# Kernel optimization log

Hardware: AMD Instinct MI355X
Metric: run time of the kernel (lower is better)

## Reference

```python
import jax, jax.numpy as jnp
import numpy as np

N_NODES = 50000
N_EDGES = 800000
IN_DIM = 32
HID = 64
OUT_DIM = 4
HEADS = 4
LAYERS = 3
N_GRAPHS = 50
NEG_SLOPE = 0.2
BN_EPS = 1e-5


def setup_inputs() -> dict:
    key = jax.random.key(0)
    ks = jax.random.split(key, 20)
    x = jax.random.normal(ks[0], (N_NODES, IN_DIM), dtype=jnp.float32)
    edge_index = jax.random.randint(ks[1], (2, N_EDGES), 0, N_NODES, dtype=jnp.int64)
    batch = jnp.sort(jax.random.randint(ks[2], (N_NODES,), 0, N_GRAPHS, dtype=jnp.int64))
    s = 0.05
    inp = {
        "x": x,
        "edge_index": edge_index,
        "batch": batch,
        "in_W": jax.random.normal(ks[3], (IN_DIM, HID), jnp.float32) * s,
        "in_b": jnp.zeros((HID,), jnp.float32),
        "gat_W": jax.random.normal(ks[4], (LAYERS, HID, HEADS * HID), jnp.float32) * s,
        "att_src": jax.random.normal(ks[5], (LAYERS, HEADS, HID), jnp.float32) * s,
        "att_dst": jax.random.normal(ks[6], (LAYERS, HEADS, HID), jnp.float32) * s,
        "gat_b": jnp.zeros((LAYERS, HID), jnp.float32),
        "bn_g": jnp.ones((LAYERS, HID), jnp.float32),
        "bn_b": jnp.zeros((LAYERS, HID), jnp.float32),
        "bn_m": jnp.zeros((LAYERS, HID), jnp.float32),
        "bn_v": jnp.ones((LAYERS, HID), jnp.float32),
        "fc1_W": jax.random.normal(ks[7], (HID, HID), jnp.float32) * s,
        "fc1_b": jnp.zeros((HID,), jnp.float32),
        "fc2_W": jax.random.normal(ks[8], (HID, OUT_DIM), jnp.float32) * s,
        "fc2_b": jnp.zeros((OUT_DIM,), jnp.float32),
    }
    return inp


def _gat_layer(x, src, dst, W, a_src, a_dst, b):
    # x: [N, HID]; src/dst: [E'] (self-loops included)
    N = x.shape[0]
    xt = (x @ W).reshape(N, HEADS, HID)           # [N, H, C]
    sc_src = jnp.einsum("nhc,hc->nh", xt, a_src)  # [N, H]
    sc_dst = jnp.einsum("nhc,hc->nh", xt, a_dst)
    e = jax.nn.leaky_relu(sc_src[src] + sc_dst[dst], NEG_SLOPE)  # [E, H]
    # segment softmax over incoming edges of each dst node
    emax = jax.ops.segment_max(e, dst, num_segments=N)
    ex = jnp.exp(e - emax[dst])
    denom = jax.ops.segment_sum(ex, dst, num_segments=N)
    alpha = ex / (denom[dst] + 1e-16)             # [E, H]
    msg = xt[src] * alpha[:, :, None]             # [E, H, C]
    out = jax.ops.segment_sum(msg, dst, num_segments=N)  # [N, H, C]
    return out.mean(axis=1) + b                   # head-average (concat=False)


def reference(x, edge_index, batch, in_W, in_b, gat_W, att_src, att_dst, gat_b,
              bn_g, bn_b, bn_m, bn_v, fc1_W, fc1_b, fc2_W, fc2_b):
    N = x.shape[0]
    loops = jnp.arange(N, dtype=edge_index.dtype)
    src = jnp.concatenate([edge_index[0], loops])
    dst = jnp.concatenate([edge_index[1], loops])

    h = x @ in_W + in_b  # dropout: eval mode (identity)
    for i in range(LAYERS):
        identity = h
        h = _gat_layer(h, src, dst, gat_W[i], att_src[i], att_dst[i], gat_b[i])
        # BatchNorm1d in eval mode (running stats)
        h = (h - bn_m[i]) * jax.lax.rsqrt(bn_v[i] + BN_EPS) * bn_g[i] + bn_b[i]
        h = jax.nn.relu(h)
        h = h + identity

    # global mean pool over graphs
    sums = jax.ops.segment_sum(h, batch, num_segments=N_GRAPHS)
    cnt = jax.ops.segment_sum(jnp.ones((N,), h.dtype), batch, num_segments=N_GRAPHS)
    g = sums / jnp.maximum(cnt, 1.0)[:, None]     # [N_GRAPHS, HID]

    g = jax.nn.relu(g @ fc1_W + fc1_b)
    return g @ fc2_W + fc2_b                      # [N_GRAPHS, OUT_DIM]
```

## Files before the change

kernel.cpp:

```cpp
#include <hip/hip_runtime.h>
#include <hip/hip_fp16.h>
#include <math.h>

#define HID 64
#define HEADS 4
#define HC 256
#define IN_DIM 32
#define NEG 0.2f
#define BN_EPS 1e-5f
#define CAP 64

typedef _Float16 f16;
typedef _Float16 f16x8 __attribute__((ext_vector_type(8)));
typedef float f32x4 __attribute__((ext_vector_type(4)));

__device__ __forceinline__ int ld_idx(const int* __restrict__ p, int i, int f64) {
    return f64 ? p[(size_t)2 * i] : p[i];
}

__global__ void k_init(const int* __restrict__ ei, int* __restrict__ flag,
                       int* __restrict__ deg, float* __restrict__ gsum,
                       int N, int NG,
                       const float* __restrict__ gat_W, const float* __restrict__ asrc,
                       const float* __restrict__ adst, float* __restrict__ wts,
                       float* __restrict__ wtd, __half* __restrict__ BT) {
    int i = blockIdx.x * blockDim.x + threadIdx.x;
    if (i == 0) {
        int z = 1;
#pragma unroll
        for (int k = 1; k < 64; k += 2) z &= (ei[k] == 0);
        *flag = z;
    }
    if (i < N) deg[i] = 0;
    if (i < NG) gsum[i] = 0.f;
    if (blockIdx.x < 3) {
        int l = blockIdx.x;
        int t = threadIdx.x;
        int hh = t >> 6, k = t & 63;
        {
            const float* W = gat_W + (size_t)l * HID * HC + (size_t)k * HC + hh * HID;
            const float* as = asrc + (size_t)l * HEADS * HID + hh * HID;
            const float* ad = adst + (size_t)l * HEADS * HID + hh * HID;
            float s1 = 0.f, s2 = 0.f;
#pragma unroll
            for (int c = 0; c < HID; ++c) { s1 += W[c] * as[c]; s2 += W[c] * ad[c]; }
            wts[l * HC + hh * HID + k] = s1;
            wtd[l * HC + hh * HID + k] = s2;
        }
        {
            int c = t & 63, jg = t >> 6;
            const float* W = gat_W + (size_t)l * HID * HC;
            __half* o = BT + (size_t)l * HID * HC + (size_t)c * HC + jg * 64;
#pragma unroll
            for (int jj = 0; jj < 64; ++jj)
                o[jj] = __float2half(W[(size_t)jj * HC + jg * 64 + c]);
        }
    }
}

__global__ void k_build(const int* __restrict__ ei, const int* __restrict__ flagp,
                        int* __restrict__ deg, unsigned short* __restrict__ src_pad,
                        int E) {
    int e = blockIdx.x * blockDim.x + threadIdx.x;
    if (e >= E) return;
    const int f = *flagp;
    int s = ld_idx(ei, e, f);
    int d = ld_idx(ei, E + e, f);
    int pos = atomicAdd(&deg[d], 1);
    if (pos < CAP) src_pad[(size_t)d * CAP + pos] = (unsigned short)s;
}

__global__ __launch_bounds__(256) void k_input(
        const float* __restrict__ x, const float* __restrict__ W,
        const float* __restrict__ b, const float* __restrict__ wts0,
        const float* __restrict__ wtd0, float* __restrict__ h,
        __half* __restrict__ h16, float* __restrict__ ssrc,
        float* __restrict__ sdst, int N) {
    int w = threadIdx.x >> 6, lane = threadIdx.x & 63;
    int n = blockIdx.x * 4 + w;
    if (n >= N) return;
    float xv = x[(size_t)n * IN_DIM + (lane & 31)];
    float acc = b[lane];
#pragma unroll
    for (int k = 0; k < IN_DIM; ++k)
        acc += __shfl(xv, k, 64) * W[k * HID + lane];
    h[(size_t)n * HID + lane] = acc;
    h16[(size_t)n * HID + lane] = __float2half(acc);
    float p0 = acc * wts0[0 * HID + lane];
    float p1 = acc * wts0[1 * HID + lane];
    float p2 = acc * wts0[2 * HID + lane];
    float p3 = acc * wts0[3 * HID + lane];
    float q0 = acc * wtd0[0 * HID + lane];
    float q1 = acc * wtd0[1 * HID + lane];
    float q2 = acc * wtd0[2 * HID + lane];
    float q3 = acc * wtd0[3 * HID + lane];
#pragma unroll
    for (int m = 32; m >= 1; m >>= 1) {
        p0 += __shfl_xor(p0, m, 64); p1 += __shfl_xor(p1, m, 64);
        p2 += __shfl_xor(p2, m, 64); p3 += __shfl_xor(p3, m, 64);
        q0 += __shfl_xor(q0, m, 64); q1 += __shfl_xor(q1, m, 64);
        q2 += __shfl_xor(q2, m, 64); q3 += __shfl_xor(q3, m, 64);
    }
    if (lane == 0) {
        *(float4*)(ssrc + (size_t)n * HEADS) = make_float4(p0, p1, p2, p3);
        *(float4*)(sdst + (size_t)n * HEADS) = make_float4(q0, q1, q2, q3);
    }
}

__global__ __launch_bounds__(256) void k_gather(
        const int* __restrict__ deg, const unsigned short* __restrict__ src_pad,
        const float* __restrict__ ssrc, const float* __restrict__ sdst,
        const __half* __restrict__ h16, __half* __restrict__ agg, int N) {
    int d = blockIdx.x * 4 + (threadIdx.x >> 6);
    if (d >= N) return;
    const int lane = threadIdx.x & 63;
    const int g = lane >> 4, l16 = lane & 15;
    const int dg = min(deg[d], CAP);
    const int se = (int)src_pad[(size_t)d * CAP + lane];
    const float4 sdd = *(const float4*)(sdst + (size_t)d * HEADS);
    float den0 = 0.f, den1 = 0.f, den2 = 0.f, den3 = 0.f;
    float a00=0.f,a01=0.f,a02=0.f,a03=0.f, a10=0.f,a11=0.f,a12=0.f,a13=0.f;
    float a20=0.f,a21=0.f,a22=0.f,a23=0.f, a30=0.f,a31=0.f,a32=0.f,a33=0.f;
    {
        float4 ssd = *(const float4*)(ssrc + (size_t)d * HEADS);
        uint2 hu = *(const uint2*)(h16 + (size_t)d * HID + l16 * 4);
        float2 f01 = __half22float2(*(__half2*)&hu.x);
        float2 f23 = __half22float2(*(__half2*)&hu.y);
        if (g == 0) {
            float v0 = ssd.x + sdd.x; v0 = v0 > 0.f ? v0 : NEG * v0;
            float v1 = ssd.y + sdd.y; v1 = v1 > 0.f ? v1 : NEG * v1;
            float v2 = ssd.z + sdd.z; v2 = v2 > 0.f ? v2 : NEG * v2;
            float v3 = ssd.w + sdd.w; v3 = v3 > 0.f ? v3 : NEG * v3;
            float e0 = __expf(v0), e1 = __expf(v1), e2 = __expf(v2), e3 = __expf(v3);
            den0 = e0; den1 = e1; den2 = e2; den3 = e3;
            a00 = e0*f01.x; a01 = e0*f01.y; a02 = e0*f23.x; a03 = e0*f23.y;
            a10 = e1*f01.x; a11 = e1*f01.y; a12 = e1*f23.x; a13 = e1*f23.y;
            a20 = e2*f01.x; a21 = e2*f01.y; a22 = e2*f23.x; a23 = e2*f23.y;
            a30 = e3*f01.x; a31 = e3*f01.y; a32 = e3*f23.x; a33 = e3*f23.y;
        }
    }
    bool vc = g < dg;
    int sc = __shfl(se, g, 64); sc = vc ? sc : d;
    float4 ss_cur = *(const float4*)(ssrc + (size_t)sc * HEADS);
    uint2  hu_cur = *(const uint2*)(h16 + (size_t)sc * HID + l16 * 4);
    for (int b = 0; b < dg; b += 4) {
        int idn = b + 4 + g;
        bool vn = idn < dg;
        int sn = __shfl(se, idn & 63, 64); sn = vn ? sn : d;
        float4 ss_nxt = *(const float4*)(ssrc + (size_t)sn * HEADS);
        uint2  hu_nxt = *(const uint2*)(h16 + (size_t)sn * HID + l16 * 4);
        float u0 = ss_cur.x + sdd.x; u0 = u0 > 0.f ? u0 : NEG * u0;
        float u1 = ss_cur.y + sdd.y; u1 = u1 > 0.f ? u1 : NEG * u1;
        float u2 = ss_cur.z + sdd.z; u2 = u2 > 0.f ? u2 : NEG * u2;
        float u3 = ss_cur.w + sdd.w; u3 = u3 > 0.f ? u3 : NEG * u3;
        float e0 = vc ? __expf(u0) : 0.f;
        float e1 = vc ? __expf(u1) : 0.f;
        float e2 = vc ? __expf(u2) : 0.f;
        float e3 = vc ? __expf(u3) : 0.f;
        float2 f01 = __half22float2(*(__half2*)&hu_cur.x);
        float2 f23 = __half22float2(*(__half2*)&hu_cur.y);
        den0 += e0; den1 += e1; den2 += e2; den3 += e3;
        a00 += e0*f01.x; a01 += e0*f01.y; a02 += e0*f23.x; a03 += e0*f23.y;
        a10 += e1*f01.x; a11 += e1*f01.y; a12 += e1*f23.x; a13 += e1*f23.y;
        a20 += e2*f01.x; a21 += e2*f01.y; a22 += e2*f23.x; a23 += e2*f23.y;
        a30 += e3*f01.x; a31 += e3*f01.y; a32 += e3*f23.x; a33 += e3*f23.y;
        ss_cur = ss_nxt; hu_cur = hu_nxt; vc = vn;
    }
#define FOLD(v) { v += __shfl_xor(v, 16, 64); v += __shfl_xor(v, 32, 64); }
    FOLD(den0) FOLD(den1) FOLD(den2) FOLD(den3)
    FOLD(a00) FOLD(a01) FOLD(a02) FOLD(a03)
    FOLD(a10) FOLD(a11) FOLD(a12) FOLD(a13)
    FOLD(a20) FOLD(a21) FOLD(a22) FOLD(a23)
    FOLD(a30) FOLD(a31) FOLD(a32) FOLD(a33)
#undef FOLD
    float iv, o0, o1, o2, o3;
    if (g == 0)      { iv = 0.25f / den0; o0 = a00; o1 = a01; o2 = a02; o3 = a03; }
    else if (g == 1) { iv = 0.25f / den1; o0 = a10; o1 = a11; o2 = a12; o3 = a13; }
    else if (g == 2) { iv = 0.25f / den2; o0 = a20; o1 = a21; o2 = a22; o3 = a23; }
    else             { iv = 0.25f / den3; o0 = a30; o1 = a31; o2 = a32; o3 = a33; }
    __half2 q01 = __floats2half2_rn(o0 * iv, o1 * iv);
    __half2 q23 = __floats2half2_rn(o2 * iv, o3 * iv);
    uint2 st;
    st.x = *(unsigned int*)&q01;
    st.y = *(unsigned int*)&q23;
    *(uint2*)(agg + ((size_t)d * HC + g * HID + l16 * 4)) = st;
}

__global__ __launch_bounds__(256) void k_postW(
        const __half* __restrict__ agg, const __half* __restrict__ BT,
        const float* __restrict__ gb, const float* __restrict__ bg,
        const float* __restrict__ bb, const float* __restrict__ bm,
        const float* __restrict__ bv, const float* __restrict__ wtsn,
        const float* __restrict__ wtdn, float* __restrict__ h,
        __half* __restrict__ h16, float* __restrict__ ssrc,
        float* __restrict__ sdst, int N) {
    __shared__ float lds[64][68];
    const int t = threadIdx.x;
    const int w = t >> 6, l = t & 63;
    const int l16 = l & 15, lk = l >> 4;
    const f16* BTf = (const f16*)BT;
    const f16* af = (const f16*)agg;
    int row = blockIdx.x * 64 + w * 16 + l16;
    int rowc = min(row, N - 1);
    f32x4 acc[4];
#pragma unroll
    for (int nt = 0; nt < 4; ++nt) acc[nt] = (f32x4){0.f, 0.f, 0.f, 0.f};
#pragma unroll
    for (int ks = 0; ks < 8; ++ks) {
        f16x8 a = *(const f16x8*)(af + (size_t)rowc * HC + ks * 32 + lk * 8);
#pragma unroll
        for (int nt = 0; nt < 4; ++nt) {
            f16x8 bfr = *(const f16x8*)(BTf + (size_t)(nt * 16 + l16) * HC + ks * 32 + lk * 8);
            acc[nt] = __builtin_amdgcn_mfma_f32_16x16x32_f16(a, bfr, acc[nt], 0, 0, 0);
        }
    }
#pragma unroll
    for (int nt = 0; nt < 4; ++nt)
#pragma unroll
        for (int r = 0; r < 4; ++r)
            lds[w * 16 + lk * 4 + r][nt * 16 + l16] = acc[nt][r];
    __syncthreads();
    {
        int j = t >> 2, q = t & 3;
        int n = blockIdx.x * 64 + j;
        if (n < N) {
            int c0 = q * 16;
            float o[16];
            float* hrow = h + (size_t)n * HID;
#pragma unroll
            for (int i4 = 0; i4 < 4; ++i4) {
                int c = c0 + i4 * 4;
                float4 sv = *(const float4*)&lds[j][c];
                float4 r4 = *(const float4*)(hrow + c);
                float4 gb4 = *(const float4*)(gb + c);
                float4 bg4 = *(const float4*)(bg + c);
                float4 bb4 = *(const float4*)(bb + c);
                float4 bm4 = *(const float4*)(bm + c);
                float4 bv4 = *(const float4*)(bv + c);
                float4 ov;
                float v;
                v = sv.x + gb4.x; v = (v - bm4.x) * rsqrtf(bv4.x + BN_EPS) * bg4.x + bb4.x;
                ov.x = fmaxf(v, 0.f) + r4.x;
                v = sv.y + gb4.y; v = (v - bm4.y) * rsqrtf(bv4.y + BN_EPS) * bg4.y + bb4.y;
                ov.y = fmaxf(v, 0.f) + r4.y;
                v = sv.z + gb4.z; v = (v - bm4.z) * rsqrtf(bv4.z + BN_EPS) * bg4.z + bb4.z;
                ov.z = fmaxf(v, 0.f) + r4.z;
                v = sv.w + gb4.w; v = (v - bm4.w) * rsqrtf(bv4.w + BN_EPS) * bg4.w + bb4.w;
                ov.w = fmaxf(v, 0.f) + r4.w;
                *(float4*)(hrow + c) = ov;
                o[i4 * 4 + 0] = ov.x; o[i4 * 4 + 1] = ov.y;
                o[i4 * 4 + 2] = ov.z; o[i4 * 4 + 3] = ov.w;
            }
            {
                __half2 hp[8];
#pragma unroll
                for (int i = 0; i < 8; ++i)
                    hp[i] = __floats2half2_rn(o[2 * i], o[2 * i + 1]);
                uint4 u0, u1;
                u0.x = *(unsigned*)&hp[0]; u0.y = *(unsigned*)&hp[1];
                u0.z = *(unsigned*)&hp[2]; u0.w = *(unsigned*)&hp[3];
                u1.x = *(unsigned*)&hp[4]; u1.y = *(unsigned*)&hp[5];
                u1.z = *(unsigned*)&hp[6]; u1.w = *(unsigned*)&hp[7];
                *(uint4*)(h16 + (size_t)n * HID + c0) = u0;
                *(uint4*)(h16 + (size_t)n * HID + c0 + 8) = u1;
            }
            if (wtsn) {
                float ps0 = 0.f, ps1 = 0.f, ps2 = 0.f, ps3 = 0.f;
                float pd0 = 0.f, pd1 = 0.f, pd2 = 0.f, pd3 = 0.f;
#pragma unroll
                for (int i = 0; i < 16; ++i) {
                    int c = c0 + i;
                    float ov = o[i];
                    ps0 += ov * wtsn[0 * HID + c]; ps1 += ov * wtsn[1 * HID + c];
                    ps2 += ov * wtsn[2 * HID + c]; ps3 += ov * wtsn[3 * HID + c];
                    pd0 += ov * wtdn[0 * HID + c]; pd1 += ov * wtdn[1 * HID + c];
                    pd2 += ov * wtdn[2 * HID + c]; pd3 += ov * wtdn[3 * HID + c];
                }
#pragma unroll
                for (int m = 2; m >= 1; m >>= 1) {
                    ps0 += __shfl_xor(ps0, m, 64); ps1 += __shfl_xor(ps1, m, 64);
                    ps2 += __shfl_xor(ps2, m, 64); ps3 += __shfl_xor(ps3, m, 64);
                    pd0 += __shfl_xor(pd0, m, 64); pd1 += __shfl_xor(pd1, m, 64);
                    pd2 += __shfl_xor(pd2, m, 64); pd3 += __shfl_xor(pd3, m, 64);
                }
                if (q == 0) {
                    *(float4*)(ssrc + (size_t)n * HEADS) = make_float4(ps0, ps1, ps2, ps3);
                    *(float4*)(sdst + (size_t)n * HEADS) = make_float4(pd0, pd1, pd2, pd3);
                }
            }
        }
    }
}

#define NPBK 64
__global__ void k_pool_sum(const float* __restrict__ h, const int* __restrict__ batch,
                           const int* __restrict__ flagp, float* __restrict__ gsum, int N) {
    const int f = *flagp;
    int c = threadIdx.x;
    int n0 = blockIdx.x * NPBK;
    int n1 = min(n0 + NPBK, N);
    if (n0 >= N) return;
    int cur = ld_idx(batch, n0, f);
    float s = 0.f;
    for (int n = n0; n < n1; ++n) {
        int g = ld_idx(batch, n, f);
        if (g != cur) {
            atomicAdd(&gsum[cur * HID + c], s);
            s = 0.f;
            cur = g;
        }
        s += h[(size_t)n * HID + c];
    }
    atomicAdd(&gsum[cur * HID + c], s);
}

__device__ __forceinline__ int lower_bound_i(const int* __restrict__ a, int n, int v, int f) {
    int lo = 0, hi = n;
    while (lo < hi) {
        int mid = (lo + hi) >> 1;
        if (ld_idx(a, mid, f) < v) lo = mid + 1; else hi = mid;
    }
    return lo;
}

__global__ void k_mlp(const float* __restrict__ gsum, const int* __restrict__ batch,
                      const int* __restrict__ flagp, int N,
                      const float* __restrict__ W1, const float* __restrict__ b1,
                      const float* __restrict__ W2, const float* __restrict__ b2,
                      float* __restrict__ out, int OUTD) {
    int gg = blockIdx.x, c = threadIdx.x;
    const int f = *flagp;
    int lo = lower_bound_i(batch, N, gg, f);
    int hi = lower_bound_i(batch, N, gg + 1, f);
    float cnt = (float)(hi - lo);
    __shared__ float gs[HID];
    __shared__ float s1[HID];
    gs[c] = gsum[gg * HID + c] / fmaxf(cnt, 1.f);
    __syncthreads();
    float acc = b1[c];
#pragma unroll
    for (int k = 0; k < HID; ++k) acc += gs[k] * W1[k * HID + c];
    s1[c] = fmaxf(acc, 0.f);
    __syncthreads();
    if (c < OUTD) {
        float o = b2[c];
#pragma unroll
        for (int k = 0; k < HID; ++k) o += s1[k] * W2[k * OUTD + c];
        out[gg * OUTD + c] = o;
    }
}

extern "C" void kernel_launch(void* const* d_in, const int* in_sizes, int n_in,
                              void* d_out, int out_size, void* d_ws, size_t ws_size,
                              hipStream_t stream) {
    const float* x       = (const float*)d_in[0];
    const int*   ei_raw  = (const int*)d_in[1];
    const int*   b_raw   = (const int*)d_in[2];
    const float* in_W    = (const float*)d_in[3];
    const float* in_b    = (const float*)d_in[4];
    const float* gat_W   = (const float*)d_in[5];
    const float* att_src = (const float*)d_in[6];
    const float* att_dst = (const float*)d_in[7];
    const float* gat_b   = (const float*)d_in[8];
    const float* bn_g    = (const float*)d_in[9];
    const float* bn_b    = (const float*)d_in[10];
    const float* bn_m    = (const float*)d_in[11];
    const float* bn_v    = (const float*)d_in[12];
    const float* fc1_W   = (const float*)d_in[13];
    const float* fc1_b   = (const float*)d_in[14];
    const float* fc2_W   = (const float*)d_in[15];
    const float* fc2_b   = (const float*)d_in[16];

    const int N = in_sizes[2];
    const int E = in_sizes[1] / 2;
    const int OUTD = 4;
    const int G = out_size / OUTD;

    float*  h    = (float*)d_ws;
    __half* h16  = (__half*)(h + (size_t)N * HID);
    __half* agg  = h16 + (size_t)N * HID;
    float*  ssrc = (float*)(agg + (size_t)N * HC);
    float*  sdst = ssrc + (size_t)N * HEADS;
    float*  wts  = sdst + (size_t)N * HEADS;
    float*  wtd  = wts + 3 * HC;
    __half* BT   = (__half*)(wtd + 3 * HC);
    float*  gsum = (float*)(BT + 3 * HID * HC);
    int*    deg  = (int*)(gsum + (size_t)G * HID);
    unsigned short* src_pad = (unsigned short*)(deg + N);
    int*    flag = (int*)(src_pad + (size_t)N * CAP);

    k_init<<<(max(N, G * HID) + 255) / 256, 256, 0, stream>>>(
        ei_raw, flag, deg, gsum, N, G * HID,
        gat_W, att_src, att_dst, wts, wtd, BT);
    k_build<<<(E + 255) / 256, 256, 0, stream>>>(ei_raw, flag, deg, src_pad, E);
    k_input<<<(N + 3) / 4, 256, 0, stream>>>(x, in_W, in_b, wts, wtd, h, h16,
                                             ssrc, sdst, N);

    for (int l = 0; l < 3; ++l) {
        k_gather<<<(N + 3) / 4, 256, 0, stream>>>(
            deg, src_pad, ssrc, sdst, h16, agg, N);
        const float* wtsn = (l < 2) ? (wts + (l + 1) * HC) : nullptr;
        const float* wtdn = (l < 2) ? (wtd + (l + 1) * HC) : nullptr;
        k_postW<<<(N + 63) / 64, 256, 0, stream>>>(
            agg, BT + (size_t)l * HID * HC,
            gat_b + (size_t)l * HID, bn_g + (size_t)l * HID, bn_b + (size_t)l * HID,
            bn_m + (size_t)l * HID, bn_v + (size_t)l * HID,
            wtsn, wtdn, h, h16, ssrc, sdst, N);
    }

    k_pool_sum<<<(N + NPBK - 1) / NPBK, HID, 0, stream>>>(h, b_raw, flag, gsum, N);
    k_mlp<<<G, HID, 0, stream>>>(gsum, b_raw, flag, N, fc1_W, fc1_b, fc2_W, fc2_b,
                                 (float*)d_out, OUTD);
}
```

Before: 328.8 us.

## Merge build and input kernels; widen gather to 8 edges per wave step

Combines the edge-bucketing kernel and the input projection into one launch, splitting roles by block index, which removes a launch and lets the two independent stages run concurrently. The gather kernel now has each wave process 8 source edges per iteration with 8 lanes each loading 16-byte half vectors, instead of 4 edges with 16 lanes loading 8 bytes. The self-loop is folded into the edge loop as slot 0 rather than handled separately. The wider split needs twice the accumulator registers and an extra shuffle-reduction level, and only half the lanes perform the store.

```diff
diff --git a/kernel.cpp b/kernel.cpp
--- a/kernel.cpp
+++ b/kernel.cpp
@@ -58,26 +58,27 @@
     }
 }
 
-__global__ void k_build(const int* __restrict__ ei, const int* __restrict__ flagp,
-                        int* __restrict__ deg, unsigned short* __restrict__ src_pad,
-                        int E) {
-    int e = blockIdx.x * blockDim.x + threadIdx.x;
-    if (e >= E) return;
-    const int f = *flagp;
-    int s = ld_idx(ei, e, f);
-    int d = ld_idx(ei, E + e, f);
-    int pos = atomicAdd(&deg[d], 1);
-    if (pos < CAP) src_pad[(size_t)d * CAP + pos] = (unsigned short)s;
-}
-
-__global__ __launch_bounds__(256) void k_input(
+__global__ __launch_bounds__(256) void k_build_input(
+        const int* __restrict__ ei, const int* __restrict__ flagp,
+        int* __restrict__ deg, unsigned short* __restrict__ src_pad, int E,
         const float* __restrict__ x, const float* __restrict__ W,
         const float* __restrict__ b, const float* __restrict__ wts0,
         const float* __restrict__ wtd0, float* __restrict__ h,
         __half* __restrict__ h16, float* __restrict__ ssrc,
-        float* __restrict__ sdst, int N) {
+        float* __restrict__ sdst, int N, int nb_build) {
+    const int f = *flagp;
+    if ((int)blockIdx.x < nb_build) {
+        int e = blockIdx.x * 256 + threadIdx.x;
+        if (e >= E) return;
+        int s = ld_idx(ei, e, f);
+        int d = ld_idx(ei, E + e, f);
+        int pos = atomicAdd(&deg[d], 1);
+        if (pos < CAP) src_pad[(size_t)d * CAP + pos] = (unsigned short)s;
+        return;
+    }
+    int blk = blockIdx.x - nb_build;
     int w = threadIdx.x >> 6, lane = threadIdx.x & 63;
-    int n = blockIdx.x * 4 + w;
+    int n = blk * 4 + w;
     if (n >= N) return;
     float xv = x[(size_t)n * IN_DIM + (lane & 31)];
     float acc = b[lane];
@@ -114,41 +115,36 @@
     int d = blockIdx.x * 4 + (threadIdx.x >> 6);
     if (d >= N) return;
     const int lane = threadIdx.x & 63;
-    const int g = lane >> 4, l16 = lane & 15;
+    const int g = lane >> 3, l8 = lane & 7;
     const int dg = min(deg[d], CAP);
+    const int tot = dg + 1;
     const int se = (int)src_pad[(size_t)d * CAP + lane];
     const float4 sdd = *(const float4*)(sdst + (size_t)d * HEADS);
     float den0 = 0.f, den1 = 0.f, den2 = 0.f, den3 = 0.f;
-    float a00=0.f,a01=0.f,a02=0.f,a03=0.f, a10=0.f,a11=0.f,a12=0.f,a13=0.f;
-    float a20=0.f,a21=0.f,a22=0.f,a23=0.f, a30=0.f,a31=0.f,a32=0.f,a33=0.f;
+    float acc0[8], acc1[8], acc2[8], acc3[8];
+#pragma unroll
+    for (int i = 0; i < 8; ++i) { acc0[i] = 0.f; acc1[i] = 0.f; acc2[i] = 0.f; acc3[i] = 0.f; }
+
+    bool vc = g < tot;
+    int sc;
     {
-        float4 ssd = *(const float4*)(ssrc + (size_t)d * HEADS);
-        uint2 hu = *(const uint2*)(h16 + (size_t)d * HID + l16 * 4);
-        float2 f01 = __half22float2(*(__half2*)&hu.x);
-        float2 f23 = __half22float2(*(__half2*)&hu.y);
-        if (g == 0) {
-            float v0 = ssd.x + sdd.x; v0 = v0 > 0.f ? v0 : NEG * v0;
-            float v1 = ssd.y + sdd.y; v1 = v1 > 0.f ? v1 : NEG * v1;
-            float v2 = ssd.z + sdd.z; v2 = v2 > 0.f ? v2 : NEG * v2;
-            float v3 = ssd.w + sdd.w; v3 = v3 > 0.f ? v3 : NEG * v3;
-            float e0 = __expf(v0), e1 = __expf(v1), e2 = __expf(v2), e3 = __expf(v3);
-            den0 = e0; den1 = e1; den2 = e2; den3 = e3;
-            a00 = e0*f01.x; a01 = e0*f01.y; a02 = e0*f23.x; a03 = e0*f23.y;
-            a10 = e1*f01.x; a11 = e1*f01.y; a12 = e1*f23.x; a13 = e1*f23.y;
-            a20 = e2*f01.x; a21 = e2*f01.y; a22 = e2*f23.x; a23 = e2*f23.y;
-            a30 = e3*f01.x; a31 = e3*f01.y; a32 = e3*f23.x; a33 = e3*f23.y;
-        }
-    }
-    bool vc = g < dg;
-    int sc = __shfl(se, g, 64); sc = vc ? sc : d;
+        int sj = __shfl(se, (g - 1) & 63, 64);
+        sc = (g == 0) ? d : sj;
+        sc = vc ? sc : d;
+    }
     float4 ss_cur = *(const float4*)(ssrc + (size_t)sc * HEADS);
-    uint2  hu_cur = *(const uint2*)(h16 + (size_t)sc * HID + l16 * 4);
-    for (int b = 0; b < dg; b += 4) {
-        int idn = b + 4 + g;
-        bool vn = idn < dg;
-        int sn = __shfl(se, idn & 63, 64); sn = vn ? sn : d;
+    uint4  hu_cur = *(const uint4*)(h16 + (size_t)sc * HID + l8 * 8);
+
+    for (int b = 0; b < tot; b += 8) {
+        int idn = b + 8 + g;
+        bool vn = idn < tot;
+        int sn;
+        {
+            int sj = __shfl(se, (idn - 1) & 63, 64);
+            sn = vn ? sj : d;
+        }
         float4 ss_nxt = *(const float4*)(ssrc + (size_t)sn * HEADS);
-        uint2  hu_nxt = *(const uint2*)(h16 + (size_t)sn * HID + l16 * 4);
+        uint4  hu_nxt = *(const uint4*)(h16 + (size_t)sn * HID + l8 * 8);
         float u0 = ss_cur.x + sdd.x; u0 = u0 > 0.f ? u0 : NEG * u0;
         float u1 = ss_cur.y + sdd.y; u1 = u1 > 0.f ? u1 : NEG * u1;
         float u2 = ss_cur.z + sdd.z; u2 = u2 > 0.f ? u2 : NEG * u2;
@@ -157,33 +153,48 @@
         float e1 = vc ? __expf(u1) : 0.f;
         float e2 = vc ? __expf(u2) : 0.f;
         float e3 = vc ? __expf(u3) : 0.f;
-        float2 f01 = __half22float2(*(__half2*)&hu_cur.x);
-        float2 f23 = __half22float2(*(__half2*)&hu_cur.y);
+        const __half2* hp = (const __half2*)&hu_cur;
+        float2 f0 = __half22float2(hp[0]);
+        float2 f1 = __half22float2(hp[1]);
+        float2 f2 = __half22float2(hp[2]);
+        float2 f3 = __half22float2(hp[3]);
+        float fv[8] = {f0.x, f0.y, f1.x, f1.y, f2.x, f2.y, f3.x, f3.y};
         den0 += e0; den1 += e1; den2 += e2; den3 += e3;
-        a00 += e0*f01.x; a01 += e0*f01.y; a02 += e0*f23.x; a03 += e0*f23.y;
-        a10 += e1*f01.x; a11 += e1*f01.y; a12 += e1*f23.x; a13 += e1*f23.y;
-        a20 += e2*f01.x; a21 += e2*f01.y; a22 += e2*f23.x; a23 += e2*f23.y;
-        a30 += e3*f01.x; a31 += e3*f01.y; a32 += e3*f23.x; a33 += e3*f23.y;
+#pragma unroll
+        for (int i = 0; i < 8; ++i) {
+            acc0[i] += e0 * fv[i];
+            acc1[i] += e1 * fv[i];
+            acc2[i] += e2 * fv[i];
+            acc3[i] += e3 * fv[i];
+        }
         ss_cur = ss_nxt; hu_cur = hu_nxt; vc = vn;
     }
-#define FOLD(v) { v += __shfl_xor(v, 16, 64); v += __shfl_xor(v, 32, 64); }
+#define FOLD(v) { v += __shfl_xor(v, 8, 64); v += __shfl_xor(v, 16, 64); v += __shfl_xor(v, 32, 64); }
     FOLD(den0) FOLD(den1) FOLD(den2) FOLD(den3)
-    FOLD(a00) FOLD(a01) FOLD(a02) FOLD(a03)
-    FOLD(a10) FOLD(a11) FOLD(a12) FOLD(a13)
-    FOLD(a20) FOLD(a21) FOLD(a22) FOLD(a23)
-    FOLD(a30) FOLD(a31) FOLD(a32) FOLD(a33)
+#pragma unroll
+    for (int i = 0; i < 8; ++i) {
+        FOLD(acc0[i]) FOLD(acc1[i]) FOLD(acc2[i]) FOLD(acc3[i])
+    }
 #undef FOLD
-    float iv, o0, o1, o2, o3;
-    if (g == 0)      { iv = 0.25f / den0; o0 = a00; o1 = a01; o2 = a02; o3 = a03; }
-    else if (g == 1) { iv = 0.25f / den1; o0 = a10; o1 = a11; o2 = a12; o3 = a13; }
-    else if (g == 2) { iv = 0.25f / den2; o0 = a20; o1 = a21; o2 = a22; o3 = a23; }
-    else             { iv = 0.25f / den3; o0 = a30; o1 = a31; o2 = a32; o3 = a33; }
-    __half2 q01 = __floats2half2_rn(o0 * iv, o1 * iv);
-    __half2 q23 = __floats2half2_rn(o2 * iv, o3 * iv);
-    uint2 st;
-    st.x = *(unsigned int*)&q01;
-    st.y = *(unsigned int*)&q23;
-    *(uint2*)(agg + ((size_t)d * HC + g * HID + l16 * 4)) = st;
+    if (lane < 32) {
+        int hh = lane >> 3;
+        float dh = hh == 0 ? den0 : hh == 1 ? den1 : hh == 2 ? den2 : den3;
+        float iv = 0.25f / dh;
+        float o[8];
+#pragma unroll
+        for (int i = 0; i < 8; ++i) {
+            float a = hh == 0 ? acc0[i] : hh == 1 ? acc1[i] : hh == 2 ? acc2[i] : acc3[i];
+            o[i] = a * iv;
+        }
+        __half2 hp0 = __floats2half2_rn(o[0], o[1]);
+        __half2 hp1 = __floats2half2_rn(o[2], o[3]);
+        __half2 hp2 = __floats2half2_rn(o[4], o[5]);
+        __half2 hp3 = __floats2half2_rn(o[6], o[7]);
+        uint4 st;
+        st.x = *(unsigned*)&hp0; st.y = *(unsigned*)&hp1;
+        st.z = *(unsigned*)&hp2; st.w = *(unsigned*)&hp3;
+        *(uint4*)(agg + ((size_t)d * HC + hh * HID + l8 * 8)) = st;
+    }
 }
 
 __global__ __launch_bounds__(256) void k_postW(
@@ -375,6 +386,8 @@
     const int E = in_sizes[1] / 2;
     const int OUTD = 4;
     const int G = out_size / OUTD;
+    const int nb_build = (E + 255) / 256;
+    const int nb_input = (N + 3) / 4;
 
     float*  h    = (float*)d_ws;
     __half* h16  = (__half*)(h + (size_t)N * HID);
@@ -392,9 +405,9 @@
     k_init<<<(max(N, G * HID) + 255) / 256, 256, 0, stream>>>(
         ei_raw, flag, deg, gsum, N, G * HID,
         gat_W, att_src, att_dst, wts, wtd, BT);
-    k_build<<<(E + 255) / 256, 256, 0, stream>>>(ei_raw, flag, deg, src_pad, E);
-    k_input<<<(N + 3) / 4, 256, 0, stream>>>(x, in_W, in_b, wts, wtd, h, h16,
-                                             ssrc, sdst, N);
+    k_build_input<<<nb_build + nb_input, 256, 0, stream>>>(
+        ei_raw, flag, deg, src_pad, E,
+        x, in_W, in_b, wts, wtd, h, h16, ssrc, sdst, N, nb_build);
 
     for (int l = 0; l < 3; ++l) {
         k_gather<<<(N + 3) / 4, 256, 0, stream>>>(
```

Measured after the change: 403.2 us. 22.6% more time.
